# Kernel optimization log

Measured on AMD Instinct MI355X. Metric: run time of the kernel, lower is better.

Reference implementation:

```python
import jax, jax.numpy as jnp
import numpy as np

N_NODES = 50000
N_EDGES = 800000
IN_CH = 128
HID = 128
N_CLASSES = 10
NUM_GRAPHS = 64


def setup_inputs() -> dict:
    key = jax.random.key(0)
    ks = jax.random.split(key, 16)
    x = jax.random.normal(ks[0], (N_NODES, IN_CH), dtype=jnp.float32)
    edge_index = jax.random.randint(ks[1], (2, N_EDGES), 0, N_NODES, dtype=jnp.int64)
    batch = jnp.sort(jax.random.randint(ks[2], (N_NODES,), 0, NUM_GRAPHS, dtype=jnp.int64))

    def lin(k, fan_in, fan_out):
        # torch nn.Linear default init: U(-1/sqrt(fan_in), 1/sqrt(fan_in))
        kw, kb = jax.random.split(k)
        bound = 1.0 / np.sqrt(fan_in)
        W = jax.random.uniform(kw, (fan_out, fan_in), jnp.float32, -bound, bound)
        b = jax.random.uniform(kb, (fan_out,), jnp.float32, -bound, bound)
        return W, b

    W_msg1, b_msg1 = lin(ks[3], IN_CH, HID)
    W_upd1, b_upd1 = lin(ks[4], IN_CH + HID, HID)
    W_msg2, b_msg2 = lin(ks[5], HID, HID)
    W_upd2, b_upd2 = lin(ks[6], HID + HID, HID)
    W_cls, b_cls = lin(ks[7], HID, N_CLASSES)
    return {
        "x": x, "edge_index": edge_index, "batch": batch,
        "W_msg1": W_msg1, "b_msg1": b_msg1, "W_upd1": W_upd1, "b_upd1": b_upd1,
        "W_msg2": W_msg2, "b_msg2": b_msg2, "W_upd2": W_upd2, "b_upd2": b_upd2,
        "W_cls": W_cls, "b_cls": b_cls,
    }


def _mpnn_layer(x, row, col, W_msg, b_msg, W_upd, b_upd):
    # gather -> linear message
    messages = x[col] @ W_msg.T + b_msg          # [E, out]
    # scatter-add aggregate into node buckets
    aggr = jax.ops.segment_sum(messages, row, num_segments=x.shape[0])  # [N, out]
    # concat + linear + ReLU update
    h = jnp.concatenate([x, aggr], axis=1) @ W_upd.T + b_upd
    return jax.nn.relu(h)


def reference(x, edge_index, batch,
              W_msg1, b_msg1, W_upd1, b_upd1,
              W_msg2, b_msg2, W_upd2, b_upd2,
              W_cls, b_cls):
    row, col = edge_index[0], edge_index[1]
    h = _mpnn_layer(x, row, col, W_msg1, b_msg1, W_upd1, b_upd1)
    h = _mpnn_layer(h, row, col, W_msg2, b_msg2, W_upd2, b_upd2)
    # mean pool per graph
    pooled = jax.ops.segment_sum(h, batch, num_segments=NUM_GRAPHS)   # [G, HID]
    count = jnp.bincount(batch, length=NUM_GRAPHS).astype(pooled.dtype)
    pooled = pooled / count[:, None]
    return pooled @ W_cls.T + b_cls
```

## Files before the change

kernel.cpp:

```cpp
#include <hip/hip_runtime.h>
#include <hip/hip_bf16.h>

#define N_NODES 50000
#define N_EDGES 800000
#define NUM_GRAPHS 64
#define NBUCK 391
#define SLAB 4096

typedef __attribute__((ext_vector_type(8))) short short8;
typedef __attribute__((ext_vector_type(16))) float f32x16;

static __device__ __forceinline__ short f2bf(float f) {
    union { __hip_bfloat16 h; short s; } u;
    u.h = __float2bfloat16(f);
    return u.s;
}
static __device__ __forceinline__ unsigned short f2bfu(float f) {
    union { __hip_bfloat16 h; unsigned short s; } u;
    u.h = __float2bfloat16(f);
    return u.s;
}
static __device__ __forceinline__ float bflo(unsigned u) { return __uint_as_float(u << 16); }
static __device__ __forceinline__ float bfhi(unsigned u) { return __uint_as_float(u & 0xffff0000u); }

__global__ __launch_bounds__(256) void prep_kernel(
    const float* __restrict__ x, uint4* __restrict__ xb,
    const float* __restrict__ Wu1, const float* __restrict__ Wm1,
    const float* __restrict__ bm1, short* __restrict__ Wcatf1, float* __restrict__ c1,
    const float* __restrict__ Wu2, const float* __restrict__ Wm2,
    const float* __restrict__ bm2, short* __restrict__ Wcatf2, float* __restrict__ c2,
    int* __restrict__ bcur, float* __restrict__ pooled) {
    int bid = blockIdx.x, t = threadIdx.x;
    if (bid < 3125) {
        int i = bid * 256 + t;
        if (i < 800000) {
            const float4* p = (const float4*)(x + (size_t)i * 8);
            float4 f0 = p[0], f1 = p[1];
            uint4 r;
            r.x = ((unsigned)f2bfu(f0.y) << 16) | f2bfu(f0.x);
            r.y = ((unsigned)f2bfu(f0.w) << 16) | f2bfu(f0.z);
            r.z = ((unsigned)f2bfu(f1.y) << 16) | f2bfu(f1.x);
            r.w = ((unsigned)f2bfu(f1.w) << 16) | f2bfu(f1.z);
            xb[i] = r;
        }
    } else if (bid < 3381) {
        int lb = bid - 3125;
        int layer = lb >> 7;
        int o = lb & 127;
        int k = t;
        const float* Wu = layer ? Wu2 : Wu1;
        const float* Wm = layer ? Wm2 : Wm1;
        const float* bm = layer ? bm2 : bm1;
        short* Wcatf = layer ? Wcatf2 : Wcatf1;
        float* cvec = layer ? c2 : c1;
        float val;
        if (k < 128) {
            val = Wu[o * 256 + k];
        } else {
            int kk = k - 128;
            float s = 0.f;
            for (int j = 0; j < 128; ++j) s += Wu[o * 256 + 128 + j] * Wm[j * 128 + kk];
            val = s;
        }
        Wcatf[(((k >> 3) * 128) + o) * 8 + (k & 7)] = f2bf(val);
        if (k == 0) {
            float cs = 0.f;
            for (int j = 0; j < 128; ++j) cs += Wu[o * 256 + 128 + j] * bm[j];
            cvec[o] = cs;
        }
    } else {
        int i = (bid - 3381) * 256 + t;
        if (i < 512) bcur[i] = i * SLAB;
        else if (i < 512 + 8192) pooled[i - 512] = 0.f;
    }
}

__global__ __launch_bounds__(1024) void binA_kernel(const int* __restrict__ row,
                                                    const int* __restrict__ col,
                                                    int* __restrict__ bcur,
                                                    unsigned* __restrict__ ebin, int E) {
    __shared__ int lcur[NBUCK];
    __shared__ int lscan[NBUCK];
    __shared__ int gbase[NBUCK];
    __shared__ int sscan[512];
    __shared__ unsigned stage[4096];
    int t = threadIdx.x;
    for (int i = t; i < NBUCK; i += 1024) lcur[i] = 0;
    __syncthreads();
    int e0 = blockIdx.x * 4096;
    unsigned pv[4];
    int pb[4], pr[4];
#pragma unroll
    for (int k = 0; k < 4; ++k) {
        int e = e0 + k * 1024 + t;
        if (e < E) {
            int r = row[e], c = col[e];
            pv[k] = ((unsigned)r << 16) | (unsigned)c;
            pb[k] = r >> 7;
            pr[k] = atomicAdd(&lcur[pb[k]], 1);
        } else {
            pb[k] = -1;
        }
    }
    __syncthreads();
    if (t < 512) sscan[t] = (t < NBUCK) ? lcur[t] : 0;
    __syncthreads();
    for (int o = 1; o < 512; o <<= 1) {
        int a = 0;
        if (t < 512 && t >= o) a = sscan[t - o];
        __syncthreads();
        if (t < 512) sscan[t] += a;
        __syncthreads();
    }
    if (t < NBUCK) lscan[t] = sscan[t] - lcur[t];
    __syncthreads();
    for (int i = t; i < NBUCK; i += 1024) {
        int c = lcur[i];
        gbase[i] = c ? atomicAdd(&bcur[i], c) : 0;
    }
#pragma unroll
    for (int k = 0; k < 4; ++k)
        if (pb[k] >= 0) stage[lscan[pb[k]] + pr[k]] = pv[k];
    __syncthreads();
    int total = E - e0;
    if (total > 4096) total = 4096;
    for (int idx = t; idx < total; idx += 1024) {
        unsigned v = stage[idx];
        int b = v >> 23;
        ebin[gbase[b] + (idx - lscan[b])] = v;
    }
}

__global__ __launch_bounds__(256) void binB_kernel(const unsigned* __restrict__ ebin,
                                                   const int* __restrict__ bcur,
                                                   int* __restrict__ csr,
                                                   int* __restrict__ hist,
                                                   int* __restrict__ off, int N) {
    __shared__ int lcnt[128];
    __shared__ int loff[128];
    __shared__ int lcur2[128];
    __shared__ int sscan[128];
    __shared__ unsigned short stage[SLAB];
    int b = blockIdx.x, t = threadIdx.x;
    int base = b * SLAB;
    int n = bcur[b] - base;
    if (n > SLAB) n = SLAB;
    if (t < 128) lcnt[t] = 0;
    __syncthreads();
    for (int idx = t; idx < n; idx += 256) {
        unsigned v = ebin[base + idx];
        atomicAdd(&lcnt[(v >> 16) & 127], 1);
    }
    __syncthreads();
    if (t < 128) sscan[t] = lcnt[t];
    __syncthreads();
    for (int o = 1; o < 128; o <<= 1) {
        int a = 0;
        if (t < 128 && t >= o) a = sscan[t - o];
        __syncthreads();
        if (t < 128) sscan[t] += a;
        __syncthreads();
    }
    if (t < 128) {
        loff[t] = sscan[t] - lcnt[t];
        lcur2[t] = sscan[t] - lcnt[t];
    }
    __syncthreads();
    for (int idx = t; idx < n; idx += 256) {
        unsigned v = ebin[base + idx];
        int lr = (v >> 16) & 127;
        int pos = atomicAdd(&lcur2[lr], 1);
        stage[pos] = (unsigned short)(v & 0xffffu);
    }
    __syncthreads();
    for (int idx = t; idx < n; idx += 256) csr[base + idx] = (int)stage[idx];
    int r0 = b * 128;
    if (t < 128 && r0 + t < N) {
        hist[r0 + t] = lcnt[t];
        off[r0 + t] = base + loff[t];
    }
}

__global__ __launch_bounds__(256) void gather_kernel(const unsigned short* __restrict__ src,
                                                     const int* __restrict__ off,
                                                     const int* __restrict__ hist,
                                                     const int* __restrict__ csr,
                                                     unsigned int* __restrict__ aggb, int N) {
    int wave = threadIdx.x >> 6, lane = threadIdx.x & 63;
    int n = blockIdx.x * 4 + wave;
    if (n >= N) return;
    int s = off[n];
    int e = s + hist[n];
    int grp = lane >> 4, sub = lane & 15;
    float a0 = 0.f, a1 = 0.f, a2 = 0.f, a3 = 0.f, a4 = 0.f, a5 = 0.f, a6 = 0.f, a7 = 0.f;
#pragma unroll 4
    for (int i = s + grp; i < e; i += 4) {
        int c = csr[i];
        uint4 v = *(const uint4*)(src + (size_t)c * 128 + sub * 8);
        a0 += bflo(v.x); a1 += bfhi(v.x);
        a2 += bflo(v.y); a3 += bfhi(v.y);
        a4 += bflo(v.z); a5 += bfhi(v.z);
        a6 += bflo(v.w); a7 += bfhi(v.w);
    }
#pragma unroll
    for (int mk = 16; mk <= 32; mk <<= 1) {
        a0 += __shfl_xor(a0, mk); a1 += __shfl_xor(a1, mk);
        a2 += __shfl_xor(a2, mk); a3 += __shfl_xor(a3, mk);
        a4 += __shfl_xor(a4, mk); a5 += __shfl_xor(a5, mk);
        a6 += __shfl_xor(a6, mk); a7 += __shfl_xor(a7, mk);
    }
    if (grp == 0) {
        uint4 r;
        r.x = ((unsigned)f2bfu(a1) << 16) | f2bfu(a0);
        r.y = ((unsigned)f2bfu(a3) << 16) | f2bfu(a2);
        r.z = ((unsigned)f2bfu(a5) << 16) | f2bfu(a4);
        r.w = ((unsigned)f2bfu(a7) << 16) | f2bfu(a6);
        ((uint4*)aggb)[(size_t)n * 16 + sub] = r;
    }
}

template <int POOL>
__global__ __launch_bounds__(512) void update_kernel(
    const void* __restrict__ xin_, const unsigned int* __restrict__ aggb,
    const int* __restrict__ hist, const float* __restrict__ cvec,
    const float* __restrict__ bupd, const short* __restrict__ Wcatf,
    unsigned int* __restrict__ houtb, float* __restrict__ pooled,
    const int* __restrict__ batch, int N) {
    __shared__ short lds_s[32768];
    const int tid = threadIdx.x;
    const int wave = tid >> 6, lane = tid & 63;
    const int l31 = lane & 31, hi = lane >> 5;

    {
        const uint4* g = (const uint4*)Wcatf;
        uint4* l4 = (uint4*)lds_s;
#pragma unroll
        for (int j = 0; j < 8; ++j) l4[j * 512 + tid] = g[j * 512 + tid];
    }
    __syncthreads();

    const int m0 = blockIdx.x * 256 + wave * 32;
    int nr = m0 + l31;
    if (nr >= N) nr = N - 1;
    f32x16 acc[4] = {};
#pragma unroll
    for (int step = 0; step < 16; ++step) {
        short8 a;
        if (step < 8) {
            a = *(const short8*)((const short*)xin_ + (size_t)nr * 128 + step * 16 + hi * 8);
        } else {
            a = *(const short8*)((const short*)aggb + (size_t)nr * 128 + (step - 8) * 16 + hi * 8);
        }
#pragma unroll
        for (int ct = 0; ct < 4; ++ct) {
            const short8 b = *(const short8*)(lds_s + (((step * 2 + hi) * 128) + ct * 32 + l31) * 8);
            acc[ct] = __builtin_amdgcn_mfma_f32_32x32x16_bf16(a, b, acc[ct], 0, 0, 0);
        }
    }
    __syncthreads();

    float dv[16];
#pragma unroll
    for (int r = 0; r < 16; ++r) {
        int row = (r & 3) + 8 * (r >> 2) + 4 * hi;
        int node = m0 + row;
        if (node >= N) node = N - 1;
        dv[r] = (float)hist[node];
    }
    short* tp = lds_s + wave * 4096;
#pragma unroll
    for (int ct = 0; ct < 4; ++ct) {
        int o = ct * 32 + l31;
        float co = cvec[o], bo = bupd[o];
#pragma unroll
        for (int r = 0; r < 16; ++r) {
            int row = (r & 3) + 8 * (r >> 2) + 4 * hi;
            float v = fmaxf(acc[ct][r] + dv[r] * co + bo, 0.f);
            tp[row * 128 + o] = f2bf(v);
        }
    }
    __syncthreads();

    if (POOL == 0) {
        const uint4* l4 = (const uint4*)tp;
#pragma unroll
        for (int j = 0; j < 8; ++j) {
            int node = m0 + j * 4 + (lane >> 4);
            if (node < N)
                ((uint4*)houtb)[(size_t)m0 * 16 + j * 64 + lane] = l4[j * 64 + lane];
        }
    } else {
        int c = tid & 127, seg = tid >> 7;
        int base = blockIdx.x * 256 + seg * 64;
        float s = 0.f;
        int gprev = -1;
        for (int i = 0; i < 64; ++i) {
            int node = base + i;
            if (node >= N) break;
            int g = batch[node];
            if (g != gprev) {
                if (gprev >= 0) atomicAdd(&pooled[gprev * 128 + c], s);
                s = 0.f;
                gprev = g;
            }
            unsigned u = (unsigned short)lds_s[(seg * 64 + i) * 128 + c];
            s += __uint_as_float(u << 16);
        }
        if (gprev >= 0) atomicAdd(&pooled[gprev * 128 + c], s);
    }
}

__global__ void final_kernel(const float* __restrict__ pooled, const int* __restrict__ batch,
                             const float* __restrict__ Wcls, const float* __restrict__ bcls,
                             float* __restrict__ out, int N) {
    __shared__ float sh[128];
    __shared__ int cntsh;
    int g = blockIdx.x;
    int t = threadIdx.x;
    if (t == 0) {
        int lo = 0, hi = N;
        while (lo < hi) { int mid = (lo + hi) >> 1; if (batch[mid] < g) lo = mid + 1; else hi = mid; }
        int start = lo;
        lo = 0; hi = N;
        while (lo < hi) { int mid = (lo + hi) >> 1; if (batch[mid] < g + 1) lo = mid + 1; else hi = mid; }
        cntsh = lo - start;
    }
    __syncthreads();
    float c = (cntsh > 0) ? (float)cntsh : 1.f;
    sh[t] = pooled[g * 128 + t] / c;
    __syncthreads();
    if (t < 10) {
        float s = bcls[t];
        for (int i = 0; i < 128; ++i) s += sh[i] * Wcls[t * 128 + i];
        out[g * 10 + t] = s;
    }
}

extern "C" void kernel_launch(void* const* d_in, const int* in_sizes, int n_in,
                              void* d_out, int out_size, void* d_ws, size_t ws_size,
                              hipStream_t stream) {
    const float* x = (const float*)d_in[0];
    const int* ei = (const int*)d_in[1];
    const int* batch = (const int*)d_in[2];
    const float* Wm1 = (const float*)d_in[3];
    const float* bm1 = (const float*)d_in[4];
    const float* Wu1 = (const float*)d_in[5];
    const float* bu1 = (const float*)d_in[6];
    const float* Wm2 = (const float*)d_in[7];
    const float* bm2 = (const float*)d_in[8];
    const float* Wu2 = (const float*)d_in[9];
    const float* bu2 = (const float*)d_in[10];
    const float* Wcls = (const float*)d_in[11];
    const float* bcls = (const float*)d_in[12];
    float* out = (float*)d_out;

    const int N = N_NODES, E = N_EDGES;
    const int* row = ei;
    const int* col = ei + E;
    const int EB = (E + 4095) / 4096;
    const int UB = (N + 255) / 256;

    int* bcur = (int*)d_ws;
    float* pooled = (float*)(bcur + 512);
    int* hist = (int*)(pooled + 8192);
    int* off = hist + 50000;
    unsigned* ebin = (unsigned*)(off + 50000);
    int* csr = (int*)(ebin + NBUCK * SLAB);
    unsigned* aggb = (unsigned*)(csr + NBUCK * SLAB);
    unsigned* h1b = aggb + 3200000;
    unsigned* xb = h1b + 3200000;
    float* c1 = (float*)(xb + 3200000);
    float* c2 = c1 + 128;
    short* Wcatf1 = (short*)(c2 + 128);
    short* Wcatf2 = Wcatf1 + 32768;

    prep_kernel<<<3415, 256, 0, stream>>>(x, (uint4*)xb, Wu1, Wm1, bm1, Wcatf1, c1,
                                          Wu2, Wm2, bm2, Wcatf2, c2, bcur, pooled);
    binA_kernel<<<EB, 1024, 0, stream>>>(row, col, bcur, ebin, E);
    binB_kernel<<<NBUCK, 256, 0, stream>>>(ebin, bcur, csr, hist, off, N);

    gather_kernel<<<(N + 3) / 4, 256, 0, stream>>>((const unsigned short*)xb, off, hist,
                                                   csr, aggb, N);
    update_kernel<0><<<UB, 512, 0, stream>>>(xb, aggb, hist, c1, bu1, Wcatf1,
                                             h1b, nullptr, nullptr, N);
    gather_kernel<<<(N + 3) / 4, 256, 0, stream>>>((const unsigned short*)h1b, off, hist,
                                                   csr, aggb, N);
    update_kernel<1><<<UB, 512, 0, stream>>>(h1b, aggb, hist, c2, bu2, Wcatf2,
                                             nullptr, pooled, batch, N);

    final_kernel<<<NUM_GRAPHS, 128, 0, stream>>>(pooled, batch, Wcls, bcls, out, N);
}
```

Measured before the change: 135.4 us.

## Sort CSR neighbors by column sub-range and widen gather blocks to 16 waves

binB now counting-sorts each row's edges by a composite key of local row and the high bits of the column index, so each row's neighbor list is ordered by source node region. Concurrently running gathers then touch nearby feature rows, which is meant to improve L2/cache locality. The scan grows to 2048 bins with a two-level per-thread plus block scan, and hist/off are derived from the scan. The gather kernel also moves to 1024-thread blocks covering 16 nodes each, which lowers the block count but may affect occupancy and scheduling granularity.

```diff
diff --git a/kernel.cpp b/kernel.cpp
--- a/kernel.cpp
+++ b/kernel.cpp
@@ -136,58 +136,67 @@
                                                    int* __restrict__ csr,
                                                    int* __restrict__ hist,
                                                    int* __restrict__ off, int N) {
-    __shared__ int lcnt[128];
-    __shared__ int loff[128];
-    __shared__ int lcur2[128];
-    __shared__ int sscan[128];
+    __shared__ int lcnt[2048];
+    __shared__ int lcur2[2048];
+    __shared__ int lscan[2048];
+    __shared__ int wsum[256];
     __shared__ unsigned short stage[SLAB];
     int b = blockIdx.x, t = threadIdx.x;
     int base = b * SLAB;
     int n = bcur[b] - base;
     if (n > SLAB) n = SLAB;
-    if (t < 128) lcnt[t] = 0;
+#pragma unroll
+    for (int i = 0; i < 8; ++i) lcnt[t + i * 256] = 0;
     __syncthreads();
     for (int idx = t; idx < n; idx += 256) {
         unsigned v = ebin[base + idx];
-        atomicAdd(&lcnt[(v >> 16) & 127], 1);
-    }
-    __syncthreads();
-    if (t < 128) sscan[t] = lcnt[t];
-    __syncthreads();
-    for (int o = 1; o < 128; o <<= 1) {
-        int a = 0;
-        if (t < 128 && t >= o) a = sscan[t - o];
+        int key = (((v >> 16) & 127) << 4) | ((v & 0xffffu) >> 12);
+        atomicAdd(&lcnt[key], 1);
+    }
+    __syncthreads();
+    int s[8], tot = 0;
+#pragma unroll
+    for (int i = 0; i < 8; ++i) { s[i] = lcnt[t * 8 + i]; tot += s[i]; }
+    wsum[t] = tot;
+    __syncthreads();
+    for (int o = 1; o < 256; o <<= 1) {
+        int a = (t >= o) ? wsum[t - o] : 0;
         __syncthreads();
-        if (t < 128) sscan[t] += a;
+        wsum[t] += a;
         __syncthreads();
     }
-    if (t < 128) {
-        loff[t] = sscan[t] - lcnt[t];
-        lcur2[t] = sscan[t] - lcnt[t];
+    int pre = wsum[t] - tot;
+#pragma unroll
+    for (int i = 0; i < 8; ++i) {
+        lscan[t * 8 + i] = pre;
+        lcur2[t * 8 + i] = pre;
+        pre += s[i];
     }
     __syncthreads();
     for (int idx = t; idx < n; idx += 256) {
         unsigned v = ebin[base + idx];
-        int lr = (v >> 16) & 127;
-        int pos = atomicAdd(&lcur2[lr], 1);
+        int key = (((v >> 16) & 127) << 4) | ((v & 0xffffu) >> 12);
+        int pos = atomicAdd(&lcur2[key], 1);
         stage[pos] = (unsigned short)(v & 0xffffu);
     }
     __syncthreads();
     for (int idx = t; idx < n; idx += 256) csr[base + idx] = (int)stage[idx];
     int r0 = b * 128;
     if (t < 128 && r0 + t < N) {
-        hist[r0 + t] = lcnt[t];
-        off[r0 + t] = base + loff[t];
-    }
-}
-
-__global__ __launch_bounds__(256) void gather_kernel(const unsigned short* __restrict__ src,
-                                                     const int* __restrict__ off,
-                                                     const int* __restrict__ hist,
-                                                     const int* __restrict__ csr,
-                                                     unsigned int* __restrict__ aggb, int N) {
+        int stt = lscan[t * 16];
+        int end = (t == 127) ? n : lscan[(t + 1) * 16];
+        hist[r0 + t] = end - stt;
+        off[r0 + t] = base + stt;
+    }
+}
+
+__global__ __launch_bounds__(1024) void gather_kernel(const unsigned short* __restrict__ src,
+                                                      const int* __restrict__ off,
+                                                      const int* __restrict__ hist,
+                                                      const int* __restrict__ csr,
+                                                      unsigned int* __restrict__ aggb, int N) {
     int wave = threadIdx.x >> 6, lane = threadIdx.x & 63;
-    int n = blockIdx.x * 4 + wave;
+    int n = blockIdx.x * 16 + wave;
     if (n >= N) return;
     int s = off[n];
     int e = s + hist[n];
@@ -359,6 +368,7 @@
     const int* col = ei + E;
     const int EB = (E + 4095) / 4096;
     const int UB = (N + 255) / 256;
+    const int GB = (N + 15) / 16;
 
     int* bcur = (int*)d_ws;
     float* pooled = (float*)(bcur + 512);
@@ -379,12 +389,12 @@
     binA_kernel<<<EB, 1024, 0, stream>>>(row, col, bcur, ebin, E);
     binB_kernel<<<NBUCK, 256, 0, stream>>>(ebin, bcur, csr, hist, off, N);
 
-    gather_kernel<<<(N + 3) / 4, 256, 0, stream>>>((const unsigned short*)xb, off, hist,
-                                                   csr, aggb, N);
+    gather_kernel<<<GB, 1024, 0, stream>>>((const unsigned short*)xb, off, hist,
+                                           csr, aggb, N);
     update_kernel<0><<<UB, 512, 0, stream>>>(xb, aggb, hist, c1, bu1, Wcatf1,
                                              h1b, nullptr, nullptr, N);
-    gather_kernel<<<(N + 3) / 4, 256, 0, stream>>>((const unsigned short*)h1b, off, hist,
-                                                   csr, aggb, N);
+    gather_kernel<<<GB, 1024, 0, stream>>>((const unsigned short*)h1b, off, hist,
+                                           csr, aggb, N);
     update_kernel<1><<<UB, 512, 0, stream>>>(h1b, aggb, hist, c2, bu2, Wcatf2,
                                              nullptr, pooled, batch, N);
 
```

New measurement: 144.2 us. +6.5%, slower.

## Split gather into four column passes with persistent grid-stride waves

Applied to the files above, without the earlier changes.

The gather kernel now runs four passes, each covering one 64-byte column slice of the feature rows and loading a single 32-bit word per lane instead of a 16-byte vector. The aim is to keep each pass's working set of source rows small enough to stay cache-resident. It also switches to a fixed grid of 2048 blocks with grid-stride waves and uses nontemporal loads and stores for the CSR indices and the output. The cost is four times as many gather instructions and CSR reads, each narrower, which may reduce memory-level parallelism.

```diff
diff --git a/kernel.cpp b/kernel.cpp
--- a/kernel.cpp
+++ b/kernel.cpp
@@ -181,41 +181,36 @@
     }
 }
 
-__global__ __launch_bounds__(256) void gather_kernel(const unsigned short* __restrict__ src,
+__global__ __launch_bounds__(256) void gather_kernel(const unsigned* __restrict__ src,
                                                      const int* __restrict__ off,
                                                      const int* __restrict__ hist,
                                                      const int* __restrict__ csr,
-                                                     unsigned int* __restrict__ aggb, int N) {
-    int wave = threadIdx.x >> 6, lane = threadIdx.x & 63;
-    int n = blockIdx.x * 4 + wave;
-    if (n >= N) return;
-    int s = off[n];
-    int e = s + hist[n];
-    int grp = lane >> 4, sub = lane & 15;
-    float a0 = 0.f, a1 = 0.f, a2 = 0.f, a3 = 0.f, a4 = 0.f, a5 = 0.f, a6 = 0.f, a7 = 0.f;
+                                                     unsigned* __restrict__ aggb, int N) {
+    const int wave = threadIdx.x >> 6, lane = threadIdx.x & 63;
+    const int grp = lane >> 4, sub = lane & 15;
+    const int wid0 = blockIdx.x * 4 + wave;
+    const int wstride = gridDim.x * 4;
+#pragma unroll
+    for (int pass = 0; pass < 4; ++pass) {
+        const unsigned* sp = src + pass * 16 + sub;
+        for (int n = wid0; n < N; n += wstride) {
+            int s = off[n];
+            int e = s + hist[n];
+            float a0 = 0.f, a1 = 0.f;
 #pragma unroll 4
-    for (int i = s + grp; i < e; i += 4) {
-        int c = csr[i];
-        uint4 v = *(const uint4*)(src + (size_t)c * 128 + sub * 8);
-        a0 += bflo(v.x); a1 += bfhi(v.x);
-        a2 += bflo(v.y); a3 += bfhi(v.y);
-        a4 += bflo(v.z); a5 += bfhi(v.z);
-        a6 += bflo(v.w); a7 += bfhi(v.w);
-    }
-#pragma unroll
-    for (int mk = 16; mk <= 32; mk <<= 1) {
-        a0 += __shfl_xor(a0, mk); a1 += __shfl_xor(a1, mk);
-        a2 += __shfl_xor(a2, mk); a3 += __shfl_xor(a3, mk);
-        a4 += __shfl_xor(a4, mk); a5 += __shfl_xor(a5, mk);
-        a6 += __shfl_xor(a6, mk); a7 += __shfl_xor(a7, mk);
-    }
-    if (grp == 0) {
-        uint4 r;
-        r.x = ((unsigned)f2bfu(a1) << 16) | f2bfu(a0);
-        r.y = ((unsigned)f2bfu(a3) << 16) | f2bfu(a2);
-        r.z = ((unsigned)f2bfu(a5) << 16) | f2bfu(a4);
-        r.w = ((unsigned)f2bfu(a7) << 16) | f2bfu(a6);
-        ((uint4*)aggb)[(size_t)n * 16 + sub] = r;
+            for (int i = s + grp; i < e; i += 4) {
+                int c = __builtin_nontemporal_load(csr + i);
+                unsigned v = sp[(size_t)c * 64];
+                a0 += bflo(v);
+                a1 += bfhi(v);
+            }
+            a0 += __shfl_xor(a0, 16); a1 += __shfl_xor(a1, 16);
+            a0 += __shfl_xor(a0, 32); a1 += __shfl_xor(a1, 32);
+            if (grp == 0) {
+                unsigned r = ((unsigned)f2bfu(a1) << 16) | f2bfu(a0);
+                __builtin_nontemporal_store(r, aggb + (size_t)n * 64 + pass * 16 + sub);
+            }
+        }
     }
 }
 
@@ -359,6 +354,7 @@
     const int* col = ei + E;
     const int EB = (E + 4095) / 4096;
     const int UB = (N + 255) / 256;
+    const int GB = 2048;
 
     int* bcur = (int*)d_ws;
     float* pooled = (float*)(bcur + 512);
@@ -379,12 +375,10 @@
     binA_kernel<<<EB, 1024, 0, stream>>>(row, col, bcur, ebin, E);
     binB_kernel<<<NBUCK, 256, 0, stream>>>(ebin, bcur, csr, hist, off, N);
 
-    gather_kernel<<<(N + 3) / 4, 256, 0, stream>>>((const unsigned short*)xb, off, hist,
-                                                   csr, aggb, N);
+    gather_kernel<<<GB, 256, 0, stream>>>(xb, off, hist, csr, aggb, N);
     update_kernel<0><<<UB, 512, 0, stream>>>(xb, aggb, hist, c1, bu1, Wcatf1,
                                              h1b, nullptr, nullptr, N);
-    gather_kernel<<<(N + 3) / 4, 256, 0, stream>>>((const unsigned short*)h1b, off, hist,
-                                                   csr, aggb, N);
+    gather_kernel<<<GB, 256, 0, stream>>>(h1b, off, hist, csr, aggb, N);
     update_kernel<1><<<UB, 512, 0, stream>>>(h1b, aggb, hist, c2, bu2, Wcatf2,
                                              nullptr, pooled, batch, N);
 
```

Result: slower. 273.1 us (+101.7%).
